# Optimization experiments

Measured on AMD Instinct MI355X. Metric: run time of the kernel, lower is better.

Reference implementation:

```python
import jax, jax.numpy as jnp
import numpy as np

B, S, D = 1, 2048, 1536
H, HD = 24, 64
WINDOW = 512
N_ANCHORS = 4
THETA = 10000.0


def _rope(x):
    # x: [B, H, S, hd] -- matches torch code applied on (B*H, S, hd) with offset=0
    hd = x.shape[-1]
    inv_freq = 1.0 / (THETA ** (jnp.arange(0, hd, 2, dtype=jnp.float32) / hd))
    t = jnp.arange(x.shape[2], dtype=jnp.float32)
    freqs = jnp.outer(t, inv_freq)                      # [S, hd//2]
    emb = jnp.concatenate([freqs, freqs], axis=-1)      # [S, hd]
    cos, sin = jnp.cos(emb), jnp.sin(emb)
    x_rot = jnp.concatenate([-x[..., hd // 2:], x[..., : hd // 2]], axis=-1)
    return x * cos + x_rot * sin


def setup_inputs() -> dict:
    key = jax.random.key(0)
    kx, km, kq, kk, kv = jax.random.split(key, 5)
    std = 0.02
    return {
        "x": jax.random.normal(kx, (B, S, D), jnp.float32),
        "spike_mask": jax.random.bernoulli(km, 0.5, (B, S)),
        "Wq": jax.random.normal(kq, (D, D), jnp.float32) * std,
        "Wk": jax.random.normal(kk, (D, D), jnp.float32) * std,
        "Wv": jax.random.normal(kv, (D, D), jnp.float32) * std,
    }


def reference(x, spike_mask, Wq, Wk, Wv):
    Bq, Sq, Dd = x.shape
    # QKV projections (nn.Linear, bias=False: y = x @ W.T), split heads -> [B, H, S, hd]
    Q = jnp.einsum('bsd,ed->bse', x, Wq).reshape(Bq, Sq, H, HD).transpose(0, 2, 1, 3)
    K = jnp.einsum('bsd,ed->bse', x, Wk).reshape(Bq, Sq, H, HD).transpose(0, 2, 1, 3)
    V = jnp.einsum('bsd,ed->bse', x, Wv).reshape(Bq, Sq, H, HD).transpose(0, 2, 1, 3)
    Q = _rope(Q)
    K = _rope(K)

    # structured mask: causal & (within window | global anchor columns)
    pos = jnp.arange(Sq)
    dist = pos[:, None] - pos[None, :]
    attn_mask = (dist >= 0) & ((dist <= WINDOW) | (pos[None, :] < N_ANCHORS))  # [S, S]

    full_mask = attn_mask[None, None] & spike_mask[:, None, None, :]  # [B,1,S,S]
    query_has_any_key = jnp.any(full_mask, axis=-1, keepdims=True)    # [B,1,S,1]
    safe_mask = full_mask | ~query_has_any_key

    scale = HD ** -0.5
    scores = jnp.einsum('bhqd,bhkd->bhqk', Q, K) * scale
    weights = jax.nn.softmax(jnp.where(safe_mask, scores, -jnp.inf), axis=-1)
    out = jnp.einsum('bhqk,bhkd->bhqd', weights, V)
    out = jnp.where(query_has_any_key, out, 0.0)

    out = out.transpose(0, 2, 1, 3).reshape(Bq, Sq, Dd)
    return out * spike_mask[..., None].astype(out.dtype)
```

## Files before the change

### kernel.cpp

```cpp
#include <hip/hip_runtime.h>
#include <cstdint>
#include <cstddef>

#define S_LEN   2048
#define D_MODEL 1536
#define NH      24
#define HDIM    64
#define WINDOW  512
#define NANCH   4

typedef __attribute__((ext_vector_type(8))) short short8;
typedef __attribute__((ext_vector_type(4))) float floatx4;

#define ASYNC_COPY16(g, l) \
    __builtin_amdgcn_global_load_lds((const __attribute__((address_space(1))) uint32_t*)(g), \
                                     (__attribute__((address_space(3))) uint32_t*)(l), 16, 0, 0)

static __device__ __forceinline__ ushort f32_to_bf16(float f) {
    uint32_t u = __float_as_uint(f);
    uint32_t r = (u + 0x7FFFu + ((u >> 16) & 1u)) >> 16;
    return (ushort)r;
}

__global__ __launch_bounds__(256) void convert_prep_kernel(
    const float* __restrict__ x,
    const float* __restrict__ wq, const float* __restrict__ wk, const float* __restrict__ wv,
    const uint8_t* __restrict__ raw,
    ushort* __restrict__ xb, ushort* __restrict__ wb,
    float* __restrict__ normf, float* __restrict__ cs,
    int xq4, int wq4) {
    const int which = blockIdx.y;
    if (which == 4) {
        if (blockIdx.x < 256) {
            int idx = blockIdx.x * 256 + threadIdx.x;
            int s = idx >> 5, i = idx & 31;
            float inv_freq = expf(-(float)i * 0.2878231366242557f);
            float c, sn;
            sincosf((float)s * inv_freq, &sn, &c);
            cs[s * 64 + i]      = c;
            cs[s * 64 + 32 + i] = sn;
            return;
        }
        if (blockIdx.x != 256) return;
        __shared__ int sh[2];
        if (threadIdx.x == 0) { sh[0] = 0; sh[1] = 0; }
        __syncthreads();
        int f = 0, nz = 0;
        for (int i = threadIdx.x; i < S_LEN; i += 256) {
            uint8_t b = raw[i];
            if ((i & 3) == 3 && b == 0x3f) f++;
            if ((i & 3) != 0 && b != 0)    nz++;
        }
        if (f)  atomicAdd(&sh[0], f);
        if (nz) atomicAdd(&sh[1], nz);
        __syncthreads();
        const int mode = (sh[0] > 0) ? 2 : ((sh[1] > 0) ? 1 : 0);
        for (int i = threadIdx.x; i < S_LEN; i += 256) {
            int v;
            if (mode == 2)      v = (((const float*)raw)[i] != 0.0f) ? 1 : 0;
            else if (mode == 1) v = raw[i] ? 1 : 0;
            else                v = (((const int*)raw)[i] != 0) ? 1 : 0;
            normf[i] = v ? 1.0f : 0.0f;
        }
        return;
    }
    const size_t w_elems = (size_t)D_MODEL * D_MODEL;
    const float* src; ushort* dst; int n4;
    if (which == 0)      { src = x;  dst = xb;               n4 = xq4; }
    else if (which == 1) { src = wq; dst = wb;               n4 = wq4; }
    else if (which == 2) { src = wk; dst = wb + w_elems;     n4 = wq4; }
    else                 { src = wv; dst = wb + 2 * w_elems; n4 = wq4; }
    int i = blockIdx.x * blockDim.x + threadIdx.x;
    if (i >= n4) return;
    float4 v = ((const float4*)src)[i];
    ushort4 o;
    o.x = f32_to_bf16(v.x);
    o.y = f32_to_bf16(v.y);
    o.z = f32_to_bf16(v.z);
    o.w = f32_to_bf16(v.w);
    ((ushort4*)dst)[i] = o;
}

__global__ __launch_bounds__(256) void gemm_qkv_kernel(
    const ushort* __restrict__ xb,
    const ushort* __restrict__ wb,
    const float*  __restrict__ cs,
    ushort* __restrict__ Qf, ushort* __restrict__ Kf, ushort* __restrict__ Vf)
{
    const int lb  = blockIdx.x;
    const int idx = (lb & 7) * 72 + (lb >> 3);
    const int z   = idx / 192;
    const int rem = idx % 192;
    const int n2  = rem >> 4;
    const int tm  = rem & 15;
    const ushort* W = wb + (size_t)z * (D_MODEL * (size_t)D_MODEL);

    __shared__ __align__(16) char smem[32768];
    ushort* As = (ushort*)smem;
    ushort* Bs = (ushort*)(smem + 16384);

    const int tid  = threadIdx.x;
    const int wave = tid >> 6;
    const int lane = tid & 63;

    const int scol = (lane & 3) * 8;
    const int arow = wave * 32 + (lane >> 2);
    const ushort* gA0 = xb + (size_t)(tm * 128 + arow) * D_MODEL + scol;
    const ushort* gA1 = gA0 + (size_t)16 * D_MODEL;
    const ushort* gB0 = W  + (size_t)(n2 * 128 + arow) * D_MODEL + scol;
    const ushort* gB1 = gB0 + (size_t)16 * D_MODEL;
    ushort* lA0 = &As[wave * 1024];
    ushort* lA1 = lA0 + 512;
    ushort* lB0 = &Bs[wave * 1024];
    ushort* lB1 = lB0 + 512;

    const int wm = (wave >> 1) * 64;
    const int wn = (wave & 1) * 64;
    const int lrow  = lane & 15;
    const int quadk = (lane >> 4) * 8;

    floatx4 acc[4][4];
#pragma unroll
    for (int i = 0; i < 4; ++i)
#pragma unroll
        for (int j = 0; j < 4; ++j)
            acc[i][j] = (floatx4){0.f, 0.f, 0.f, 0.f};

    for (int kt = 0; kt < D_MODEL / 64; ++kt) {
        __syncthreads();
        ASYNC_COPY16(gA0 + kt * 64, lA0);
        ASYNC_COPY16(gA1 + kt * 64, lA1);
        ASYNC_COPY16(gB0 + kt * 64, lB0);
        ASYNC_COPY16(gB1 + kt * 64, lB1);
        ASYNC_COPY16(gA0 + kt * 64 + 32, lA0 + 4096);
        ASYNC_COPY16(gA1 + kt * 64 + 32, lA1 + 4096);
        ASYNC_COPY16(gB0 + kt * 64 + 32, lB0 + 4096);
        ASYNC_COPY16(gB1 + kt * 64 + 32, lB1 + 4096);
        __syncthreads();

#pragma unroll
        for (int hh = 0; hh < 2; ++hh) {
            const ushort* Ah = As + hh * 4096;
            const ushort* Bh = Bs + hh * 4096;
            short8 af[4], bf[4];
#pragma unroll
            for (int i = 0; i < 4; ++i) af[i] = *(const short8*)(&Ah[(wm + i * 16 + lrow) * 32 + quadk]);
#pragma unroll
            for (int j = 0; j < 4; ++j) bf[j] = *(const short8*)(&Bh[(wn + j * 16 + lrow) * 32 + quadk]);
#pragma unroll
            for (int i = 0; i < 4; ++i)
#pragma unroll
                for (int j = 0; j < 4; ++j)
                    acc[i][j] = __builtin_amdgcn_mfma_f32_16x16x32_bf16(af[i], bf[j], acc[i][j], 0, 0, 0);
        }
    }

    __syncthreads();
    ushort* Lw = (ushort*)(smem + wave * 5120);

    const int r0 = (lane >> 4) * 4;
    const int c0 = lane & 15;
    const int quad = lane >> 4;
    const int l16  = lane & 15;
    const int h  = n2 * 2 + (wave & 1);
    const int s0 = tm * 128 + wm;

    if (z < 2) {
        const float qscale = (z == 0) ? 0.18033688011112042f : 1.0f;
        ushort* O = (z == 0) ? Qf : Kf;
#pragma unroll
        for (int cc = 0; cc < 2; ++cc) {
#pragma unroll
            for (int i2 = 0; i2 < 2; ++i2) {
                const int i = cc * 2 + i2;
#pragma unroll
                for (int jj = 0; jj < 2; ++jj) {
                    const int cl = jj * 16 + c0;
#pragma unroll
                    for (int r = 0; r < 4; ++r) {
                        const int row = s0 + i * 16 + r0 + r;
                        const float c  = cs[row * 64 + cl];
                        const float sn = cs[row * 64 + 32 + cl];
                        const float x0 = acc[i][jj][r];
                        const float x1 = acc[i][jj + 2][r];
                        const int rl = i2 * 16 + r0 + r;
                        Lw[rl * 72 + cl]      = f32_to_bf16((x0 * c - x1 * sn) * qscale);
                        Lw[rl * 72 + cl + 32] = f32_to_bf16((x1 * c + x0 * sn) * qscale);
                    }
                }
            }
            const int t16base = tm * 8 + (wave >> 1) * 4 + cc * 2;
#pragma unroll
            for (int t = 0; t < 2; ++t) {
#pragma unroll
                for (int p = 0; p < 2; ++p) {
                    uint4 v = *(uint4*)&Lw[(t * 16 + l16) * 72 + p * 32 + quad * 8];
                    *(uint4*)&O[((((size_t)h * 128 + t16base + t) * 2 + p) * 64 + lane) * 8] = v;
                }
            }
        }
    } else {
#pragma unroll
        for (int cc = 0; cc < 2; ++cc) {
#pragma unroll
            for (int i2 = 0; i2 < 2; ++i2) {
                const int i = cc * 2 + i2;
#pragma unroll
                for (int j = 0; j < 4; ++j) {
                    const int dl = j * 16 + c0;
                    ushort4 o;
                    o.x = f32_to_bf16(acc[i][j][0]);
                    o.y = f32_to_bf16(acc[i][j][1]);
                    o.z = f32_to_bf16(acc[i][j][2]);
                    o.w = f32_to_bf16(acc[i][j][3]);
                    *(ushort4*)&Lw[dl * 40 + i2 * 16 + r0] = o;
                }
            }
            const int kc = tm * 4 + (wave >> 1) * 2 + cc;
#pragma unroll
            for (int j2 = 0; j2 < 4; ++j2) {
                uint4 v = *(uint4*)&Lw[(j2 * 16 + l16) * 40 + quad * 8];
                *(uint4*)&Vf[((((size_t)h * 64 + kc) * 4 + j2) * 64 + lane) * 8] = v;
            }
        }
    }
}

__global__ __launch_bounds__(256) void flash_attn_kernel(
    const ushort* __restrict__ Qf,
    const ushort* __restrict__ Kf,
    const ushort* __restrict__ Vf,
    const float* __restrict__ spikef,
    float* __restrict__ out)
{
    const int lb   = blockIdx.x + (blockIdx.y << 7);
    const int h    = (lb & 7) * 3 + ((lb >> 3) >> 7);
    const int qt16 = (lb >> 3) & 127;
    const int qs   = qt16 * 16;
    const int tid  = threadIdx.x;
    const int wid  = tid >> 6;
    const int lane = tid & 63;
    const int quad = lane >> 4;
    const int l16  = lane & 15;

    __shared__ __align__(16) char smem[4 * 4608];
    char* wreg = smem + wid * 4608;
    ushort* Pst = (ushort*)wreg;

    const ushort* Qp = Qf + (((size_t)h * 128 + qt16) * 2) * 512 + lane * 8;
    const short8 qf0 = *(const short8*)(Qp);
    const short8 qf1 = *(const short8*)(Qp + 512);

    const int q_lane = qs + l16;

    float lsum = 0.f;
    floatx4 Oacc[4];
#pragma unroll
    for (int j2 = 0; j2 < 4; ++j2) Oacc[j2] = (floatx4){0.f, 0.f, 0.f, 0.f};

    const int qtt = (qs + 15) >> 6;
    const int lo = (qs > WINDOW ? qs - WINDOW : 0) >> 6;
    const int has_anchor = (lo > 0) ? 1 : 0;
    const int nt = (qtt - lo + 1) + has_anchor;

    const ushort* Kh = Kf + ((size_t)h * 128) * 1024 + lane * 8;
    const ushort* Vh = Vf + ((size_t)h * 64) * 2048 + lane * 8;

    for (int it = wid; it < nt; it += 4) {
        const int t = has_anchor ? (it == 0 ? 0 : lo + it - 1) : it;
        const int mode = (t == qtt) ? 1 : ((has_anchor && t == 0) ? 3 :
                         ((qs + 15 - t * 64 > WINDOW) ? 2 : 0));

        floatx4 S[4];
        float4 sp[4];
#pragma unroll
        for (int f = 0; f < 4; ++f) {
            const int t16 = t * 4 + f;
            const ushort* Kp = Kh + (size_t)t16 * 1024;
            short8 kf0 = *(const short8*)(Kp);
            short8 kf1 = *(const short8*)(Kp + 512);
            sp[f] = *(const float4*)(spikef + t16 * 16 + quad * 4);
            floatx4 a = (floatx4){0.f, 0.f, 0.f, 0.f};
            a = __builtin_amdgcn_mfma_f32_16x16x32_bf16(kf0, qf0, a, 0, 0, 0);
            a = __builtin_amdgcn_mfma_f32_16x16x32_bf16(kf1, qf1, a, 0, 0, 0);
            S[f] = a;
        }

#pragma unroll
        for (int f = 0; f < 4; ++f) {
            const int kb = t * 64 + f * 16 + quad * 4;
#pragma unroll
            for (int r = 0; r < 4; ++r) {
                const int k = kb + r;
                float v;
                if (mode == 0)      v = 1.f;
                else if (mode == 1) v = (k <= q_lane) ? 1.f : 0.f;
                else if (mode == 2) v = ((k >= q_lane - WINDOW) || (k < NANCH)) ? 1.f : 0.f;
                else                v = (k < NANCH) ? 1.f : 0.f;
                const float sv = (r == 0) ? sp[f].x : (r == 1) ? sp[f].y : (r == 2) ? sp[f].z : sp[f].w;
                const float w = exp2f(S[f][r]) * v * sv;
                S[f][r] = w;
                lsum += w;
            }
        }

#pragma unroll
        for (int f = 0; f < 4; ++f) {
            uint32_t p01 = (__float_as_uint(S[f][0]) >> 16) | (__float_as_uint(S[f][1]) & 0xFFFF0000u);
            uint32_t p23 = (__float_as_uint(S[f][2]) >> 16) | (__float_as_uint(S[f][3]) & 0xFFFF0000u);
            uint2 pk; pk.x = p01; pk.y = p23;
            *(uint2*)(Pst + l16 * 72 + f * 16 + quad * 4) = pk;
        }

#pragma unroll
        for (int c = 0; c < 2; ++c) {
            const short8 pA = *(const short8*)(Pst + l16 * 72 + c * 32 + quad * 8);
            const int kc = t * 2 + c;
#pragma unroll
            for (int j2 = 0; j2 < 4; ++j2) {
                const short8 vf = *(const short8*)(Vh + (size_t)kc * 2048 + j2 * 512);
                Oacc[j2] = __builtin_amdgcn_mfma_f32_16x16x32_bf16(pA, vf, Oacc[j2], 0, 0, 0);
            }
        }
    }

#pragma unroll
    for (int j2 = 0; j2 < 4; ++j2)
        *(floatx4*)(wreg + j2 * 1024 + lane * 16) = Oacc[j2];
    *(float*)(wreg + 4096 + lane * 4) = lsum;
    __syncthreads();

    floatx4 Os = (floatx4){0.f, 0.f, 0.f, 0.f};
    float lt = 0.f;
#pragma unroll
    for (int w = 0; w < 4; ++w) {
        Os += *(const floatx4*)(smem + w * 4608 + wid * 1024 + lane * 16);
        lt += *(const float*)(smem + w * 4608 + 4096 + lane * 4);
    }
    lt += __shfl_xor(lt, 16);
    lt += __shfl_xor(lt, 32);

#pragma unroll
    for (int r = 0; r < 4; ++r) {
        const float lr = __int_as_float(__builtin_amdgcn_ds_bpermute((quad * 4 + r) * 4,
                                                                     __float_as_int(lt)));
        const int qrow = qs + quad * 4 + r;
        const float linv = (lr > 0.f && spikef[qrow] != 0.f) ? (1.0f / lr) : 0.f;
        out[(size_t)qrow * D_MODEL + h * HDIM + wid * 16 + l16] = Os[r] * linv;
    }
}

extern "C" void kernel_launch(void* const* d_in, const int* in_sizes, int n_in,
                              void* d_out, int out_size, void* d_ws, size_t ws_size,
                              hipStream_t stream) {
    const float* x     = (const float*)d_in[0];
    const uint8_t* spike_raw = (const uint8_t*)d_in[1];
    const float* Wq    = (const float*)d_in[2];
    const float* Wk    = (const float*)d_in[3];
    const float* Wv    = (const float*)d_in[4];
    float* out = (float*)d_out;

    const size_t xb_elems = (size_t)S_LEN * D_MODEL;
    const size_t w_elems  = (size_t)D_MODEL * D_MODEL;
    const size_t hs_elems = (size_t)NH * S_LEN * HDIM;

    char* ws = (char*)d_ws;
    size_t off = 0;
    ushort* xb = (ushort*)(ws + off); off += xb_elems * 2;
    ushort* wb = (ushort*)(ws + off); off += 3 * w_elems * 2;
    ushort* Qf = (ushort*)(ws + off); off += hs_elems * 2;
    ushort* Kf = (ushort*)(ws + off); off += hs_elems * 2;
    ushort* Vf = (ushort*)(ws + off); off += hs_elems * 2;
    float*  cst = (float*)(ws + off); off += (size_t)S_LEN * 64 * 4;
    float* spike_f = (float*)(ws + off); off += S_LEN * 4;
    if (ws_size < off) return;

    {
        int xq4 = (int)(xb_elems / 4);
        int wq4 = (int)(w_elems / 4);
        convert_prep_kernel<<<dim3(3072, 5), 256, 0, stream>>>(
            x, Wq, Wk, Wv, spike_raw, xb, wb, spike_f, cst, xq4, wq4);
    }

    gemm_qkv_kernel<<<576, 256, 0, stream>>>(xb, wb, cst, Qf, Kf, Vf);

    flash_attn_kernel<<<dim3(128, 24), 256, 0, stream>>>(Qf, Kf, Vf, spike_f, out);
}
```

Before: 189.7 us.

## Double-buffer QKV GEMM LDS tiles and XOR-swizzle to avoid bank conflicts

The QKV projection GEMM now splits each 64-wide K step into 32-wide stages held in two LDS buffers. The async global-to-LDS copy of the next stage is issued before the MFMA work on the current stage, which cuts the barrier count per stage from two to one. It also XOR-swizzles the k-column chunk on both the store and the fragment read to reduce LDS bank conflicts. The trade-off is twice as many loop iterations with smaller work each, plus an extra barrier in the epilogue.

```diff
diff --git a/kernel.cpp b/kernel.cpp
--- a/kernel.cpp
+++ b/kernel.cpp
@@ -96,28 +96,23 @@
     const ushort* W = wb + (size_t)z * (D_MODEL * (size_t)D_MODEL);
 
     __shared__ __align__(16) char smem[32768];
-    ushort* As = (ushort*)smem;
-    ushort* Bs = (ushort*)(smem + 16384);
 
     const int tid  = threadIdx.x;
     const int wave = tid >> 6;
     const int lane = tid & 63;
 
-    const int scol = (lane & 3) * 8;
+    const int scol = ((lane & 3) ^ ((lane >> 3) & 3)) * 8;
     const int arow = wave * 32 + (lane >> 2);
     const ushort* gA0 = xb + (size_t)(tm * 128 + arow) * D_MODEL + scol;
     const ushort* gA1 = gA0 + (size_t)16 * D_MODEL;
     const ushort* gB0 = W  + (size_t)(n2 * 128 + arow) * D_MODEL + scol;
     const ushort* gB1 = gB0 + (size_t)16 * D_MODEL;
-    ushort* lA0 = &As[wave * 1024];
-    ushort* lA1 = lA0 + 512;
-    ushort* lB0 = &Bs[wave * 1024];
-    ushort* lB1 = lB0 + 512;
 
     const int wm = (wave >> 1) * 64;
     const int wn = (wave & 1) * 64;
     const int lrow  = lane & 15;
-    const int quadk = (lane >> 4) * 8;
+    const int quad  = lane >> 4;
+    const int xq = (quad ^ ((lrow >> 1) & 3)) * 8;
 
     floatx4 acc[4][4];
 #pragma unroll
@@ -126,41 +121,48 @@
         for (int j = 0; j < 4; ++j)
             acc[i][j] = (floatx4){0.f, 0.f, 0.f, 0.f};
 
-    for (int kt = 0; kt < D_MODEL / 64; ++kt) {
+    auto STAGE = [&](int b, int kt) {
+        ushort* lA = (ushort*)(smem + b * 16384) + wave * 1024;
+        ushort* lB = lA + 4096;
+        const int ko = kt * 32;
+        ASYNC_COPY16(gA0 + ko, lA);
+        ASYNC_COPY16(gA1 + ko, lA + 512);
+        ASYNC_COPY16(gB0 + ko, lB);
+        ASYNC_COPY16(gB1 + ko, lB + 512);
+    };
+
+    auto COMPUTE = [&](int b) {
+        const ushort* Ah = (const ushort*)(smem + b * 16384);
+        const ushort* Bh = Ah + 4096;
+        short8 af[4], bf[4];
+#pragma unroll
+        for (int i = 0; i < 4; ++i) af[i] = *(const short8*)(&Ah[(wm + i * 16 + lrow) * 32 + xq]);
+#pragma unroll
+        for (int j = 0; j < 4; ++j) bf[j] = *(const short8*)(&Bh[(wn + j * 16 + lrow) * 32 + xq]);
+#pragma unroll
+        for (int i = 0; i < 4; ++i)
+#pragma unroll
+            for (int j = 0; j < 4; ++j)
+                acc[i][j] = __builtin_amdgcn_mfma_f32_16x16x32_bf16(af[i], bf[j], acc[i][j], 0, 0, 0);
+    };
+
+    STAGE(0, 0);
+    __syncthreads();
+
+    int cur = 0;
+    for (int kt = 0; kt < D_MODEL / 32 - 1; ++kt) {
+        STAGE(cur ^ 1, kt + 1);
+        COMPUTE(cur);
         __syncthreads();
-        ASYNC_COPY16(gA0 + kt * 64, lA0);
-        ASYNC_COPY16(gA1 + kt * 64, lA1);
-        ASYNC_COPY16(gB0 + kt * 64, lB0);
-        ASYNC_COPY16(gB1 + kt * 64, lB1);
-        ASYNC_COPY16(gA0 + kt * 64 + 32, lA0 + 4096);
-        ASYNC_COPY16(gA1 + kt * 64 + 32, lA1 + 4096);
-        ASYNC_COPY16(gB0 + kt * 64 + 32, lB0 + 4096);
-        ASYNC_COPY16(gB1 + kt * 64 + 32, lB1 + 4096);
-        __syncthreads();
-
-#pragma unroll
-        for (int hh = 0; hh < 2; ++hh) {
-            const ushort* Ah = As + hh * 4096;
-            const ushort* Bh = Bs + hh * 4096;
-            short8 af[4], bf[4];
-#pragma unroll
-            for (int i = 0; i < 4; ++i) af[i] = *(const short8*)(&Ah[(wm + i * 16 + lrow) * 32 + quadk]);
-#pragma unroll
-            for (int j = 0; j < 4; ++j) bf[j] = *(const short8*)(&Bh[(wn + j * 16 + lrow) * 32 + quadk]);
-#pragma unroll
-            for (int i = 0; i < 4; ++i)
-#pragma unroll
-                for (int j = 0; j < 4; ++j)
-                    acc[i][j] = __builtin_amdgcn_mfma_f32_16x16x32_bf16(af[i], bf[j], acc[i][j], 0, 0, 0);
-        }
-    }
+        cur ^= 1;
+    }
+    COMPUTE(cur);
 
     __syncthreads();
     ushort* Lw = (ushort*)(smem + wave * 5120);
 
     const int r0 = (lane >> 4) * 4;
     const int c0 = lane & 15;
-    const int quad = lane >> 4;
     const int l16  = lane & 15;
     const int h  = n2 * 2 + (wave & 1);
     const int s0 = tm * 128 + wm;
@@ -198,6 +200,7 @@
                     *(uint4*)&O[((((size_t)h * 128 + t16base + t) * 2 + p) * 64 + lane) * 8] = v;
                 }
             }
+            if (cc == 0) __syncthreads();
         }
     } else {
 #pragma unroll
@@ -222,6 +225,7 @@
                 uint4 v = *(uint4*)&Lw[(j2 * 16 + l16) * 40 + quad * 8];
                 *(uint4*)&Vf[((((size_t)h * 64 + kc) * 4 + j2) * 64 + lane) * 8] = v;
             }
+            if (cc == 0) __syncthreads();
         }
     }
 }
```

New measurement: 176.9 us. 1.07x faster.
